# Performance work log

Measured on AMD Instinct MI355X. Metric: run time of the kernel, lower is better.

## Reference

```python
import jax, jax.numpy as jnp
import numpy as np

N = 50000      # nodes
E = 640000     # edges
FIN = 100      # raw node feature dim (nn.Linear(100, d_model))
D = 128        # d_model (dim_hidden)
H = 8          # num_heads
DH = D // H    # head dim
L = 4          # num_layers
DFF = 4 * D    # dim_feedforward
G = 64         # number of graphs in the batch
SCALE = DH ** -0.5


def setup_inputs() -> dict:
    key = jax.random.key(0)
    ks = jax.random.split(key, 12)
    x = jax.random.normal(ks[0], (N, FIN), jnp.float32)
    edge_index = jax.random.randint(ks[1], (2, E), 0, N, dtype=jnp.int64)
    batch = jnp.sort(jax.random.randint(ks[2], (N,), 0, G, dtype=jnp.int64))

    def w(k, shape, fan_in):
        return jax.random.normal(k, shape, jnp.float32) * (fan_in ** -0.5)

    W_embed = w(ks[3], (FIN, D), FIN)          # embedding, bias=False
    Wqk = w(ks[4], (L, D, 2 * D), D)           # to_qk, bias=False
    Wv = w(ks[5], (L, D, D), D)                # to_v, bias=False
    Wout = w(ks[6], (L, D, D), D)              # out_proj
    b_out = jnp.zeros((L, D), jnp.float32)
    W1 = w(ks[7], (L, D, DFF), D)              # FFN linear1
    b1 = jnp.zeros((L, DFF), jnp.float32)
    W2 = w(ks[8], (L, DFF, D), DFF)            # FFN linear2
    b2 = jnp.zeros((L, D), jnp.float32)
    return dict(x=x, edge_index=edge_index, batch=batch, W_embed=W_embed,
                Wqk=Wqk, Wv=Wv, Wout=Wout, b_out=b_out, W1=W1, b1=b1,
                W2=W2, b2=b2)


def reference(x, edge_index, batch, W_embed, Wqk, Wv, Wout, b_out, W1, b1, W2, b2):
    src = edge_index[0]  # j (message source)
    dst = edge_index[1]  # i (aggregation target)
    h = x @ W_embed  # [N, D]; dropout is identity at eval
    for l in range(L):
        # --- DAG multi-head attention (PyG MessagePassing, aggr='add') ---
        qk = h @ Wqk[l]
        q, k = qk[:, :D], qk[:, D:]
        v = h @ Wv[l]
        qj = q[src].reshape(E, H, DH)   # qk_j: gathered at source
        ki = k[dst].reshape(E, H, DH)   # qk_i: gathered at target
        logits = (qj * ki).sum(-1) * SCALE  # [E, H]
        # segment softmax over edges sharing the same target node
        m = jax.ops.segment_max(logits, dst, num_segments=N)        # [N, H]
        p = jnp.exp(logits - m[dst])
        ssum = jax.ops.segment_sum(p, dst, num_segments=N)          # [N, H]
        attn = p / ssum[dst]
        msg = (v[src].reshape(E, H, DH) * attn[:, :, None]).reshape(E, D)
        agg = jax.ops.segment_sum(msg, dst, num_segments=N)         # [N, D]
        h = h + (agg @ Wout[l] + b_out[l])   # residual; norm1 = Identity
        # --- FFN (relu) ---
        ff = jax.nn.relu(h @ W1[l] + b1[l]) @ W2[l] + b2[l]
        h = h + ff                            # residual; norm2 = Identity
    # global mean pool over graphs
    cnt = jax.ops.segment_sum(jnp.ones((N,), h.dtype), batch, num_segments=G)
    pooled = jax.ops.segment_sum(h, batch, num_segments=G) / jnp.maximum(cnt, 1.0)[:, None]
    return pooled
```

## Files before the change

### kernel.cpp

```cpp
#include <hip/hip_runtime.h>
#include <hip/hip_bf16.h>
#include <math.h>

#define D 128
#define NH 8
#define DFF 512
#define NG 64
#define NL 4
#define FIN 100
#define SCALE 0.25f
#define QKV 384

typedef __attribute__((ext_vector_type(8))) short short8;
typedef __attribute__((ext_vector_type(4))) float f32x4;

__device__ inline unsigned short f2bf(float v) {
    __hip_bfloat16 b = __float2bfloat16(v);
    return *reinterpret_cast<unsigned short*>(&b);
}

__global__ void count_kernel(const int* __restrict__ dst, int* __restrict__ cnt, int E) {
    int e = blockIdx.x * 256 + threadIdx.x;
    if (e < E) atomicAdd(&cnt[dst[e]], 1);
}

__global__ __launch_bounds__(1024) void scan_block_kernel(const int* __restrict__ cnt,
        int* __restrict__ incl, int* __restrict__ partials, int n) {
    __shared__ int s[1024];
    int tid = threadIdx.x;
    int gid = blockIdx.x * 1024 + tid;
    int val = (gid < n) ? cnt[gid] : 0;
    s[tid] = val;
    __syncthreads();
    for (int o = 1; o < 1024; o <<= 1) {
        int t = (tid >= o) ? s[tid - o] : 0;
        __syncthreads();
        s[tid] += t;
        __syncthreads();
    }
    if (gid < n) incl[gid] = s[tid];
    if (tid == 1023) partials[blockIdx.x] = s[1023];
}

__global__ void scan_partials_kernel(int* __restrict__ partials, int nb) {
    if (threadIdx.x == 0 && blockIdx.x == 0) {
        int run = 0;
        for (int i = 0; i < nb; ++i) { int t = partials[i]; partials[i] = run; run += t; }
    }
}

__global__ void finalize_off_kernel(const int* __restrict__ cnt, const int* __restrict__ incl,
        const int* __restrict__ partials, int* __restrict__ off, int* __restrict__ cur,
        int n, int E) {
    int gid = blockIdx.x * 256 + threadIdx.x;
    if (gid < n) {
        int v = incl[gid] - cnt[gid] + partials[gid >> 10];
        off[gid] = v;
        cur[gid] = v;
    }
    if (gid == 0) off[n] = E;
}

__global__ void scatter_kernel(const int* __restrict__ src, const int* __restrict__ dst,
        int* __restrict__ cur, int* __restrict__ csr_src, int E) {
    int e = blockIdx.x * 256 + threadIdx.x;
    if (e < E) {
        int p = atomicAdd(&cur[dst[e]], 1);
        csr_src[p] = src[e];
    }
}

__global__ void transpose_cvt_kernel(const float* __restrict__ W, __hip_bfloat16* __restrict__ Bt,
        int K, int N, int ldl) {
    int l = blockIdx.y;
    const float* w = W + (size_t)l * K * N;
    __hip_bfloat16* bt = Bt + (size_t)l * ldl;
    int idx = blockIdx.x * 256 + threadIdx.x;
    if (idx >= K * N) return;
    int n = idx / K, k = idx - n * K;
    bt[(size_t)n * K + k] = __float2bfloat16(w[(size_t)k * N + n]);
}

__global__ void pad_cvt_x_kernel(const float* __restrict__ x, __hip_bfloat16* __restrict__ xb, int n) {
    int idx = blockIdx.x * 256 + threadIdx.x;
    if (idx >= n * 128) return;
    int r = idx >> 7, c = idx & 127;
    xb[idx] = (c < FIN) ? __float2bfloat16(x[(size_t)r * FIN + c]) : __float2bfloat16(0.f);
}

__global__ void wembT_kernel(const float* __restrict__ W, __hip_bfloat16* __restrict__ Bt) {
    int idx = blockIdx.x * 256 + threadIdx.x;
    if (idx >= 128 * 128) return;
    int n = idx >> 7, k = idx & 127;
    Bt[idx] = (k < FIN) ? __float2bfloat16(W[(size_t)k * 128 + n]) : __float2bfloat16(0.f);
}

template<int EPI>
__global__ __launch_bounds__(256) void gemm_mfma(
        const __hip_bfloat16* __restrict__ A, const __hip_bfloat16* __restrict__ Bt,
        const float* __restrict__ bias,
        float* __restrict__ Cf, __hip_bfloat16* __restrict__ Cb,
        int M, int N, int K) {
    __shared__ __align__(16) unsigned short As[128][64];
    __shared__ __align__(16) unsigned short Bs[64][64];
    int t = threadIdx.x;
    int wave = t >> 6, lane = t & 63;
    int row0 = blockIdx.x * 128, col0 = blockIdx.y * 64;
    f32x4 acc[2][4] = {};

    int sr = t >> 3;
    int sc = t & 7;

    for (int k0 = 0; k0 < K; k0 += 64) {
#pragma unroll
        for (int i = 0; i < 4; ++i) {
            int r = i * 32 + sr;
            int gr = row0 + r;
            if (gr >= M) gr = M - 1;
            *reinterpret_cast<short8*>(&As[r][(sc ^ (r & 7)) << 3]) =
                *reinterpret_cast<const short8*>(&A[(size_t)gr * K + k0 + (sc << 3)]);
        }
#pragma unroll
        for (int i = 0; i < 2; ++i) {
            int r = i * 32 + sr;
            *reinterpret_cast<short8*>(&Bs[r][(sc ^ (r & 7)) << 3]) =
                *reinterpret_cast<const short8*>(&Bt[(size_t)(col0 + r) * K + k0 + (sc << 3)]);
        }
        __syncthreads();
#pragma unroll
        for (int kk = 0; kk < 64; kk += 32) {
            int lr = lane & 15;
            int kc = (kk >> 3) + (lane >> 4);
            short8 a[2], b[4];
#pragma unroll
            for (int m = 0; m < 2; ++m) {
                int r = wave * 32 + m * 16 + lr;
                a[m] = *reinterpret_cast<const short8*>(&As[r][(kc ^ (r & 7)) << 3]);
            }
#pragma unroll
            for (int n = 0; n < 4; ++n) {
                int r = n * 16 + lr;
                b[n] = *reinterpret_cast<const short8*>(&Bs[r][(kc ^ (r & 7)) << 3]);
            }
#pragma unroll
            for (int m = 0; m < 2; ++m)
#pragma unroll
                for (int n = 0; n < 4; ++n)
                    acc[m][n] = __builtin_amdgcn_mfma_f32_16x16x32_bf16(a[m], b[n], acc[m][n], 0, 0, 0);
        }
        __syncthreads();
    }

    int lr = lane & 15, rg = (lane >> 4) * 4;
#pragma unroll
    for (int m = 0; m < 2; ++m) {
#pragma unroll
        for (int n = 0; n < 4; ++n) {
            int col = col0 + n * 16 + lr;
#pragma unroll
            for (int j = 0; j < 4; ++j) {
                int row = row0 + wave * 32 + m * 16 + rg + j;
                if (row < M) {
                    float val = acc[m][n][j];
                    Cf[(size_t)row * N + col] = val;
                    Cb[(size_t)row * N + col] = __float2bfloat16(val);
                }
            }
        }
    }
}

__global__ __launch_bounds__(256, 3) void gemm_qkv(
        const __hip_bfloat16* __restrict__ A, const __hip_bfloat16* __restrict__ Bt,
        __hip_bfloat16* __restrict__ Cb, int M) {
    __shared__ __align__(16) unsigned short As[128 * 128];
    __shared__ __align__(16) unsigned short Bs[64 * 128];
    int t = threadIdx.x;
    int wave = t >> 6, lane = t & 63;
    int lr = lane & 15, lg = lane >> 4;
    int row0 = blockIdx.x * 128;

#pragma unroll
    for (int i = 0; i < 8; ++i) {
        int idx = t + i * 256;
        int r = idx >> 4, ch = idx & 15;
        int gr = row0 + r; if (gr >= M) gr = M - 1;
        *reinterpret_cast<short8*>(&As[r * 128 + ((ch ^ (r & 7)) << 3)]) =
            *reinterpret_cast<const short8*>(&A[(size_t)gr * 128 + ch * 8]);
    }

    short8 a_all[2][4];
    for (int c = 0; c < 6; ++c) {
#pragma unroll
        for (int i = 0; i < 4; ++i) {
            int idx = t + i * 256;
            int r = idx >> 4, ch = idx & 15;
            *reinterpret_cast<short8*>(&Bs[r * 128 + ((ch ^ (r & 7)) << 3)]) =
                *reinterpret_cast<const short8*>(&Bt[((size_t)(c * 64 + r)) * 128 + ch * 8]);
        }
        __syncthreads();
        if (c == 0) {
#pragma unroll
            for (int m = 0; m < 2; ++m)
#pragma unroll
                for (int ks = 0; ks < 4; ++ks) {
                    int r = wave * 32 + m * 16 + lr;
                    int kc = ks * 4 + lg;
                    a_all[m][ks] = *reinterpret_cast<const short8*>(&As[r * 128 + ((kc ^ (r & 7)) << 3)]);
                }
        }
        f32x4 acc[2][4] = {};
#pragma unroll
        for (int ks = 0; ks < 4; ++ks) {
            int kc = ks * 4 + lg;
            short8 b[4];
#pragma unroll
            for (int n = 0; n < 4; ++n) {
                int r = n * 16 + lr;
                b[n] = *reinterpret_cast<const short8*>(&Bs[r * 128 + ((kc ^ (r & 7)) << 3)]);
            }
#pragma unroll
            for (int m = 0; m < 2; ++m)
#pragma unroll
                for (int n = 0; n < 4; ++n)
                    acc[m][n] = __builtin_amdgcn_mfma_f32_16x16x32_bf16(a_all[m][ks], b[n], acc[m][n], 0, 0, 0);
        }
#pragma unroll
        for (int m = 0; m < 2; ++m)
#pragma unroll
            for (int n = 0; n < 4; ++n) {
                int col = c * 64 + n * 16 + lr;
#pragma unroll
                for (int j = 0; j < 4; ++j) {
                    int row = row0 + wave * 32 + m * 16 + lg * 4 + j;
                    if (row < M)
                        Cb[(size_t)row * QKV + col] = __float2bfloat16(acc[m][n][j]);
                }
            }
        __syncthreads();
    }
}

__global__ __launch_bounds__(256, 2) void fused_out_ffn(
        const __hip_bfloat16* __restrict__ aggb, const __hip_bfloat16* __restrict__ WoutT,
        const float* __restrict__ b_out,
        const __hip_bfloat16* __restrict__ W1T, const float* __restrict__ b1,
        const __hip_bfloat16* __restrict__ W2T, const float* __restrict__ b2,
        float* __restrict__ h32, __hip_bfloat16* __restrict__ hb, int M) {
    __shared__ __align__(16) unsigned short smem[32768];
    unsigned short* As   = smem;
    unsigned short* Bs   = smem + 16384;
    unsigned short* W1s  = smem;
    unsigned short* ff1s = smem + 8192;
    unsigned short* W2s  = smem + 16384;

    int t = threadIdx.x;
    int wave = t >> 6, lane = t & 63;
    int lr = lane & 15, lg = lane >> 4;
    int row0 = blockIdx.x * 128;

#pragma unroll
    for (int i = 0; i < 8; ++i) {
        int idx = t + i * 256;
        int r = idx >> 4, ch = idx & 15;
        int gr = row0 + r; if (gr >= M) gr = M - 1;
        *reinterpret_cast<short8*>(&As[r * 128 + ((ch ^ (r & 7)) << 3)]) =
            *reinterpret_cast<const short8*>(&aggb[(size_t)gr * 128 + ch * 8]);
        *reinterpret_cast<short8*>(&Bs[r * 128 + ((ch ^ (r & 7)) << 3)]) =
            *reinterpret_cast<const short8*>(&WoutT[(size_t)r * 128 + ch * 8]);
    }
    __syncthreads();

    f32x4 acc1[2][8] = {};
#pragma unroll
    for (int ks = 0; ks < 4; ++ks) {
        int kc = ks * 4 + lg;
        short8 a[2], b[8];
#pragma unroll
        for (int m = 0; m < 2; ++m) {
            int r = wave * 32 + m * 16 + lr;
            a[m] = *reinterpret_cast<const short8*>(&As[r * 128 + ((kc ^ (r & 7)) << 3)]);
        }
#pragma unroll
        for (int n = 0; n < 8; ++n) {
            int r = n * 16 + lr;
            b[n] = *reinterpret_cast<const short8*>(&Bs[r * 128 + ((kc ^ (r & 7)) << 3)]);
        }
#pragma unroll
        for (int m = 0; m < 2; ++m)
#pragma unroll
            for (int n = 0; n < 8; ++n)
                acc1[m][n] = __builtin_amdgcn_mfma_f32_16x16x32_bf16(a[m], b[n], acc1[m][n], 0, 0, 0);
    }

#pragma unroll
    for (int m = 0; m < 2; ++m) {
#pragma unroll
        for (int n = 0; n < 8; ++n) {
            int col = n * 16 + lr;
            float bo = b_out[col];
#pragma unroll
            for (int j = 0; j < 4; ++j) {
                int rl = wave * 32 + m * 16 + lg * 4 + j;
                int row = row0 + rl;
                float hv = (row < M) ? h32[(size_t)row * 128 + col] : 0.f;
                float val = acc1[m][n][j] + bo + hv;
                acc1[m][n][j] = val;
                float other = __shfl_xor(val, 1);
                if (!(lane & 1)) {
                    unsigned lo16 = f2bf(val), hi16 = f2bf(other);
                    int ch = col >> 3;
                    int addr = rl * 128 + ((ch ^ (rl & 7)) << 3) + (col & 7);
                    *reinterpret_cast<unsigned*>(&As[addr]) = lo16 | (hi16 << 16);
                }
            }
        }
    }

    short8 a_ff[2][4];
#pragma unroll
    for (int m = 0; m < 2; ++m)
#pragma unroll
        for (int ks = 0; ks < 4; ++ks) {
            int r = wave * 32 + m * 16 + lr;
            int kc = ks * 4 + lg;
            a_ff[m][ks] = *reinterpret_cast<const short8*>(&As[r * 128 + ((kc ^ (r & 7)) << 3)]);
        }
    __syncthreads();

    f32x4 h2acc[2][8] = {};
    for (int c = 0; c < 8; ++c) {
#pragma unroll
        for (int i = 0; i < 4; ++i) {
            int idx = t + i * 256;
            int r = idx >> 4, ch = idx & 15;
            *reinterpret_cast<short8*>(&W1s[r * 128 + ((ch ^ (r & 7)) << 3)]) =
                *reinterpret_cast<const short8*>(&W1T[((size_t)(c * 64 + r)) * 128 + ch * 8]);
        }
#pragma unroll
        for (int i = 0; i < 4; ++i) {
            int idx = t + i * 256;
            int r = idx >> 3, ch = idx & 7;
            *reinterpret_cast<short8*>(&W2s[r * 64 + ((ch ^ (r & 7)) << 3)]) =
                *reinterpret_cast<const short8*>(&W2T[(size_t)r * 512 + c * 64 + ch * 8]);
        }
        __syncthreads();

        f32x4 acc2[2][4] = {};
#pragma unroll
        for (int ks = 0; ks < 4; ++ks) {
            int kc = ks * 4 + lg;
            short8 b[4];
#pragma unroll
            for (int n = 0; n < 4; ++n) {
                int r = n * 16 + lr;
                b[n] = *reinterpret_cast<const short8*>(&W1s[r * 128 + ((kc ^ (r & 7)) << 3)]);
            }
#pragma unroll
            for (int m = 0; m < 2; ++m)
#pragma unroll
                for (int n = 0; n < 4; ++n)
                    acc2[m][n] = __builtin_amdgcn_mfma_f32_16x16x32_bf16(a_ff[m][ks], b[n], acc2[m][n], 0, 0, 0);
        }
#pragma unroll
        for (int m = 0; m < 2; ++m) {
#pragma unroll
            for (int n = 0; n < 4; ++n) {
                int col = n * 16 + lr;
                float bb = b1[c * 64 + col];
#pragma unroll
                for (int j = 0; j < 4; ++j) {
                    int rl = wave * 32 + m * 16 + lg * 4 + j;
                    float val = fmaxf(acc2[m][n][j] + bb, 0.f);
                    float other = __shfl_xor(val, 1);
                    if (!(lane & 1)) {
                        unsigned lo16 = f2bf(val), hi16 = f2bf(other);
                        int ch = col >> 3;
                        int addr = rl * 64 + ((ch ^ (rl & 7)) << 3) + (col & 7);
                        *reinterpret_cast<unsigned*>(&ff1s[addr]) = lo16 | (hi16 << 16);
                    }
                }
            }
        }
#pragma unroll
        for (int ks = 0; ks < 2; ++ks) {
            int kc = ks * 4 + lg;
            short8 a2[2], b[8];
#pragma unroll
            for (int m = 0; m < 2; ++m) {
                int r = wave * 32 + m * 16 + lr;
                a2[m] = *reinterpret_cast<const short8*>(&ff1s[r * 64 + ((kc ^ (r & 7)) << 3)]);
            }
#pragma unroll
            for (int n = 0; n < 8; ++n) {
                int r = n * 16 + lr;
                b[n] = *reinterpret_cast<const short8*>(&W2s[r * 64 + ((kc ^ (r & 7)) << 3)]);
            }
#pragma unroll
            for (int m = 0; m < 2; ++m)
#pragma unroll
                for (int n = 0; n < 8; ++n)
                    h2acc[m][n] = __builtin_amdgcn_mfma_f32_16x16x32_bf16(a2[m], b[n], h2acc[m][n], 0, 0, 0);
        }
        __syncthreads();
    }

#pragma unroll
    for (int m = 0; m < 2; ++m) {
#pragma unroll
        for (int n = 0; n < 8; ++n) {
            int col = n * 16 + lr;
            float bb = b2[col];
#pragma unroll
            for (int j = 0; j < 4; ++j) {
                int row = row0 + wave * 32 + m * 16 + lg * 4 + j;
                if (row < M) {
                    float val = acc1[m][n][j] + h2acc[m][n][j] + bb;
                    h32[(size_t)row * 128 + col] = val;
                    hb[(size_t)row * 128 + col] = __float2bfloat16(val);
                }
            }
        }
    }
}

__global__ __launch_bounds__(256) void attn_kernel(const __hip_bfloat16* __restrict__ qkvb,
        const int* __restrict__ off, const int* __restrict__ csr_src,
        __hip_bfloat16* __restrict__ aggb, int n) {
    int wave = threadIdx.x >> 6;
    int lane = threadIdx.x & 63;
    int i = blockIdx.x * 4 + wave;
    if (i >= n) return;
    const unsigned* qv = reinterpret_cast<const unsigned*>(qkvb);
    unsigned ku = qv[(size_t)i * 192 + 64 + lane];
    float kx = __uint_as_float(ku << 16);
    float ky = __uint_as_float(ku & 0xffff0000u);
    int e0 = off[i], e1 = off[i + 1];
    float m = -INFINITY, ssum = 0.f, ax = 0.f, ay = 0.f;
    int e = e0;
    for (; e + 4 <= e1; e += 4) {
        int s0 = csr_src[e], s1 = csr_src[e + 1], s2 = csr_src[e + 2], s3 = csr_src[e + 3];
        unsigned q0 = qv[(size_t)s0 * 192 + lane];
        unsigned q1 = qv[(size_t)s1 * 192 + lane];
        unsigned q2 = qv[(size_t)s2 * 192 + lane];
        unsigned q3 = qv[(size_t)s3 * 192 + lane];
        unsigned w0 = qv[(size_t)s0 * 192 + 128 + lane];
        unsigned w1 = qv[(size_t)s1 * 192 + 128 + lane];
        unsigned w2 = qv[(size_t)s2 * 192 + 128 + lane];
        unsigned w3 = qv[(size_t)s3 * 192 + 128 + lane];
        float l0 = __uint_as_float(q0 << 16) * kx + __uint_as_float(q0 & 0xffff0000u) * ky;
        float l1 = __uint_as_float(q1 << 16) * kx + __uint_as_float(q1 & 0xffff0000u) * ky;
        float l2 = __uint_as_float(q2 << 16) * kx + __uint_as_float(q2 & 0xffff0000u) * ky;
        float l3 = __uint_as_float(q3 << 16) * kx + __uint_as_float(q3 & 0xffff0000u) * ky;
        l0 += __shfl_xor(l0, 1); l1 += __shfl_xor(l1, 1); l2 += __shfl_xor(l2, 1); l3 += __shfl_xor(l3, 1);
        l0 += __shfl_xor(l0, 2); l1 += __shfl_xor(l1, 2); l2 += __shfl_xor(l2, 2); l3 += __shfl_xor(l3, 2);
        l0 += __shfl_xor(l0, 4); l1 += __shfl_xor(l1, 4); l2 += __shfl_xor(l2, 4); l3 += __shfl_xor(l3, 4);
        l0 *= SCALE; l1 *= SCALE; l2 *= SCALE; l3 *= SCALE;
        float mx = fmaxf(fmaxf(l0, l1), fmaxf(l2, l3));
        float mn = fmaxf(m, mx);
        float corr = __expf(m - mn);
        float p0 = __expf(l0 - mn);
        float p1 = __expf(l1 - mn);
        float p2 = __expf(l2 - mn);
        float p3 = __expf(l3 - mn);
        ssum = ssum * corr + ((p0 + p1) + (p2 + p3));
        ax = ax * corr + p0 * __uint_as_float(w0 << 16) + p1 * __uint_as_float(w1 << 16)
                       + p2 * __uint_as_float(w2 << 16) + p3 * __uint_as_float(w3 << 16);
        ay = ay * corr + p0 * __uint_as_float(w0 & 0xffff0000u) + p1 * __uint_as_float(w1 & 0xffff0000u)
                       + p2 * __uint_as_float(w2 & 0xffff0000u) + p3 * __uint_as_float(w3 & 0xffff0000u);
        m = mn;
    }
    for (; e < e1; ++e) {
        int s0 = csr_src[e];
        unsigned q0 = qv[(size_t)s0 * 192 + lane];
        unsigned w0 = qv[(size_t)s0 * 192 + 128 + lane];
        float l0 = __uint_as_float(q0 << 16) * kx + __uint_as_float(q0 & 0xffff0000u) * ky;
// ... 69 lines not shown

    int Nn = in_sizes[2];
    int E = in_sizes[1] / 2;

    char* p = (char*)d_ws;
    auto alloc = [&](size_t bytes) {
        char* r = p;
        p += (bytes + 255) & ~(size_t)255;
        return r;
    };
    float* h32 = (float*)alloc((size_t)Nn * D * 4);
    __hip_bfloat16* hb = (__hip_bfloat16*)alloc((size_t)Nn * D * 2);
    __hip_bfloat16* aggb = (__hip_bfloat16*)alloc((size_t)Nn * D * 2);
    __hip_bfloat16* qkvb = (__hip_bfloat16*)alloc((size_t)Nn * QKV * 2);
    __hip_bfloat16* xb = (__hip_bfloat16*)alloc((size_t)Nn * D * 2);
    __hip_bfloat16* WembT = (__hip_bfloat16*)alloc((size_t)D * D * 2);
    __hip_bfloat16* WqkvT = (__hip_bfloat16*)alloc((size_t)NL * QKV * D * 2);
    __hip_bfloat16* WoutT = (__hip_bfloat16*)alloc((size_t)NL * D * D * 2);
    __hip_bfloat16* W1T = (__hip_bfloat16*)alloc((size_t)NL * D * DFF * 2);
    __hip_bfloat16* W2T = (__hip_bfloat16*)alloc((size_t)NL * DFF * D * 2);
    int* csr_src = (int*)alloc((size_t)E * 4);
    int* cnt = (int*)alloc((size_t)Nn * 4);
    int* incl = (int*)alloc((size_t)Nn * 4);
    int* off = (int*)alloc(((size_t)Nn + 1) * 4);
    int* cur = (int*)alloc((size_t)Nn * 4);
    int* partials = (int*)alloc(1024 * 4);
    int* gstart = (int*)alloc((NG + 1) * 4);
    float* pws = (float*)alloc((size_t)NG * 8 * 128 * 4);

    const int* e_src = ei;
    const int* e_dst = ei + E;

    hipMemsetAsync(cnt, 0, (size_t)Nn * 4, stream);
    count_kernel<<<(E + 255) / 256, 256, 0, stream>>>(e_dst, cnt, E);
    int nsb = (Nn + 1023) / 1024;
    scan_block_kernel<<<nsb, 1024, 0, stream>>>(cnt, incl, partials, Nn);
    scan_partials_kernel<<<1, 64, 0, stream>>>(partials, nsb);
    finalize_off_kernel<<<(Nn + 255) / 256, 256, 0, stream>>>(cnt, incl, partials, off, cur, Nn, E);
    scatter_kernel<<<(E + 255) / 256, 256, 0, stream>>>(e_src, e_dst, cur, csr_src, E);

    transpose_cvt_kernel<<<dim3((2 * D * D + 255) / 256, NL), 256, 0, stream>>>(
        Wqk, WqkvT, D, 2 * D, QKV * D);
    transpose_cvt_kernel<<<dim3((D * D + 255) / 256, NL), 256, 0, stream>>>(
        Wv, WqkvT + (size_t)2 * D * D, D, D, QKV * D);
    transpose_cvt_kernel<<<dim3((D * D + 255) / 256, NL), 256, 0, stream>>>(
        Wout, WoutT, D, D, D * D);
    transpose_cvt_kernel<<<dim3((D * DFF + 255) / 256, NL), 256, 0, stream>>>(
        W1, W1T, D, DFF, D * DFF);
    transpose_cvt_kernel<<<dim3((DFF * D + 255) / 256, NL), 256, 0, stream>>>(
        W2, W2T, DFF, D, DFF * D);
    wembT_kernel<<<(128 * 128 + 255) / 256, 256, 0, stream>>>(W_embed, WembT);
    pad_cvt_x_kernel<<<((size_t)Nn * 128 + 255) / 256, 256, 0, stream>>>(x, xb, Nn);

    int gmb = (Nn + 127) / 128;
    gemm_mfma<3><<<dim3(gmb, D / 64), 256, 0, stream>>>(
        xb, WembT, nullptr, h32, hb, Nn, D, D);

    for (int l = 0; l < NL; ++l) {
        gemm_qkv<<<gmb, 256, 0, stream>>>(hb, WqkvT + (size_t)l * QKV * D, qkvb, Nn);
        attn_kernel<<<(Nn + 3) / 4, 256, 0, stream>>>(qkvb, off, csr_src, aggb, Nn);
        fused_out_ffn<<<gmb, 256, 0, stream>>>(
            aggb, WoutT + (size_t)l * D * D, b_out + (size_t)l * D,
            W1T + (size_t)l * D * DFF, b1 + (size_t)l * DFF,
            W2T + (size_t)l * DFF * D, b2 + (size_t)l * D,
            h32, hb, Nn);
    }

    group_bounds_kernel<<<1, 128, 0, stream>>>(batch, Nn, gstart);
    pool_stage1<<<dim3(NG, 8), 256, 0, stream>>>(h32, gstart, pws);
    pool_stage2<<<NG, 128, 0, stream>>>(pws, gstart, (float*)d_out);
}
```

Measured before the change: 700.4 us.

## Load GEMM operands directly from global memory, dropping LDS staging and block syncs

The embed, QKV and fused out-proj/FFN GEMMs now load A and B fragments straight from global memory into registers instead of staging tiles in shared memory behind __syncthreads. The FFN keeps only small per-wave LDS buffers for re-layout and synchronises with s_waitcnt rather than block barriers. It also drops the separate h2acc accumulator by accumulating into acc1, which lowers register pressure and removes the min-blocks launch bound. The goal is to remove barrier stalls and LDS traffic. The cost is redundant global and L2 reads of the weights by every wave, plus uncoalesced fragment loads.

```diff
diff --git a/kernel.cpp b/kernel.cpp
--- a/kernel.cpp
+++ b/kernel.cpp
@@ -95,135 +95,80 @@
     Bt[idx] = (k < FIN) ? __float2bfloat16(W[(size_t)k * 128 + n]) : __float2bfloat16(0.f);
 }
 
-template<int EPI>
-__global__ __launch_bounds__(256) void gemm_mfma(
+__global__ __launch_bounds__(256) void embed_kernel(
         const __hip_bfloat16* __restrict__ A, const __hip_bfloat16* __restrict__ Bt,
-        const float* __restrict__ bias,
-        float* __restrict__ Cf, __hip_bfloat16* __restrict__ Cb,
-        int M, int N, int K) {
-    __shared__ __align__(16) unsigned short As[128][64];
-    __shared__ __align__(16) unsigned short Bs[64][64];
-    int t = threadIdx.x;
-    int wave = t >> 6, lane = t & 63;
-    int row0 = blockIdx.x * 128, col0 = blockIdx.y * 64;
-    f32x4 acc[2][4] = {};
-
-    int sr = t >> 3;
-    int sc = t & 7;
-
-    for (int k0 = 0; k0 < K; k0 += 64) {
-#pragma unroll
-        for (int i = 0; i < 4; ++i) {
-            int r = i * 32 + sr;
-            int gr = row0 + r;
-            if (gr >= M) gr = M - 1;
-            *reinterpret_cast<short8*>(&As[r][(sc ^ (r & 7)) << 3]) =
-                *reinterpret_cast<const short8*>(&A[(size_t)gr * K + k0 + (sc << 3)]);
-        }
-#pragma unroll
-        for (int i = 0; i < 2; ++i) {
-            int r = i * 32 + sr;
-            *reinterpret_cast<short8*>(&Bs[r][(sc ^ (r & 7)) << 3]) =
-                *reinterpret_cast<const short8*>(&Bt[(size_t)(col0 + r) * K + k0 + (sc << 3)]);
-        }
-        __syncthreads();
-#pragma unroll
-        for (int kk = 0; kk < 64; kk += 32) {
-            int lr = lane & 15;
-            int kc = (kk >> 3) + (lane >> 4);
-            short8 a[2], b[4];
-#pragma unroll
-            for (int m = 0; m < 2; ++m) {
-                int r = wave * 32 + m * 16 + lr;
-                a[m] = *reinterpret_cast<const short8*>(&As[r][(kc ^ (r & 7)) << 3]);
-            }
-#pragma unroll
-            for (int n = 0; n < 4; ++n) {
-                int r = n * 16 + lr;
-                b[n] = *reinterpret_cast<const short8*>(&Bs[r][(kc ^ (r & 7)) << 3]);
-            }
-#pragma unroll
-            for (int m = 0; m < 2; ++m)
-#pragma unroll
-                for (int n = 0; n < 4; ++n)
-                    acc[m][n] = __builtin_amdgcn_mfma_f32_16x16x32_bf16(a[m], b[n], acc[m][n], 0, 0, 0);
-        }
-        __syncthreads();
-    }
-
-    int lr = lane & 15, rg = (lane >> 4) * 4;
-#pragma unroll
-    for (int m = 0; m < 2; ++m) {
-#pragma unroll
-        for (int n = 0; n < 4; ++n) {
-            int col = col0 + n * 16 + lr;
-#pragma unroll
-            for (int j = 0; j < 4; ++j) {
-                int row = row0 + wave * 32 + m * 16 + rg + j;
-                if (row < M) {
-                    float val = acc[m][n][j];
-                    Cf[(size_t)row * N + col] = val;
-                    Cb[(size_t)row * N + col] = __float2bfloat16(val);
-                }
-            }
-        }
-    }
-}
-
-__global__ __launch_bounds__(256, 3) void gemm_qkv(
-        const __hip_bfloat16* __restrict__ A, const __hip_bfloat16* __restrict__ Bt,
-        __hip_bfloat16* __restrict__ Cb, int M) {
-    __shared__ __align__(16) unsigned short As[128 * 128];
-    __shared__ __align__(16) unsigned short Bs[64 * 128];
+        float* __restrict__ h32, __hip_bfloat16* __restrict__ hb, int M) {
     int t = threadIdx.x;
     int wave = t >> 6, lane = t & 63;
     int lr = lane & 15, lg = lane >> 4;
-    int row0 = blockIdx.x * 128;
-
-#pragma unroll
-    for (int i = 0; i < 8; ++i) {
-        int idx = t + i * 256;
-        int r = idx >> 4, ch = idx & 15;
-        int gr = row0 + r; if (gr >= M) gr = M - 1;
-        *reinterpret_cast<short8*>(&As[r * 128 + ((ch ^ (r & 7)) << 3)]) =
-            *reinterpret_cast<const short8*>(&A[(size_t)gr * 128 + ch * 8]);
-    }
-
-    short8 a_all[2][4];
+    int row0 = blockIdx.x * 128 + wave * 32;
+    f32x4 acc[2][8] = {};
+#pragma unroll
+    for (int ks = 0; ks < 4; ++ks) {
+        int kc = ks * 4 + lg;
+        short8 a[2], b[8];
+#pragma unroll
+        for (int m = 0; m < 2; ++m) {
+            int gr = row0 + m * 16 + lr; if (gr >= M) gr = M - 1;
+            a[m] = *reinterpret_cast<const short8*>(&A[(size_t)gr * 128 + kc * 8]);
+        }
+#pragma unroll
+        for (int n = 0; n < 8; ++n)
+            b[n] = *reinterpret_cast<const short8*>(&Bt[(size_t)(n * 16 + lr) * 128 + kc * 8]);
+#pragma unroll
+        for (int m = 0; m < 2; ++m)
+#pragma unroll
+            for (int n = 0; n < 8; ++n)
+                acc[m][n] = __builtin_amdgcn_mfma_f32_16x16x32_bf16(a[m], b[n], acc[m][n], 0, 0, 0);
+    }
+#pragma unroll
+    for (int m = 0; m < 2; ++m)
+#pragma unroll
+        for (int n = 0; n < 8; ++n) {
+            int col = n * 16 + lr;
+#pragma unroll
+            for (int j = 0; j < 4; ++j) {
+                int row = row0 + m * 16 + lg * 4 + j;
+                if (row < M) {
+                    float val = acc[m][n][j];
+                    h32[(size_t)row * 128 + col] = val;
+                    hb[(size_t)row * 128 + col] = __float2bfloat16(val);
+                }
+            }
+        }
+}
+
+__global__ __launch_bounds__(256) void gemm_qkv(
+        const __hip_bfloat16* __restrict__ A, const __hip_bfloat16* __restrict__ Bt,
+        __hip_bfloat16* __restrict__ Cb, int M) {
+    int t = threadIdx.x;
+    int wave = t >> 6, lane = t & 63;
+    int lr = lane & 15, lg = lane >> 4;
+    int row0 = blockIdx.x * 128 + wave * 32;
+
+    short8 a[2][4];
+#pragma unroll
+    for (int m = 0; m < 2; ++m)
+#pragma unroll
+        for (int ks = 0; ks < 4; ++ks) {
+            int gr = row0 + m * 16 + lr; if (gr >= M) gr = M - 1;
+            a[m][ks] = *reinterpret_cast<const short8*>(&A[(size_t)gr * 128 + (ks * 4 + lg) * 8]);
+        }
+
     for (int c = 0; c < 6; ++c) {
-#pragma unroll
-        for (int i = 0; i < 4; ++i) {
-            int idx = t + i * 256;
-            int r = idx >> 4, ch = idx & 15;
-            *reinterpret_cast<short8*>(&Bs[r * 128 + ((ch ^ (r & 7)) << 3)]) =
-                *reinterpret_cast<const short8*>(&Bt[((size_t)(c * 64 + r)) * 128 + ch * 8]);
-        }
-        __syncthreads();
-        if (c == 0) {
-#pragma unroll
-            for (int m = 0; m < 2; ++m)
-#pragma unroll
-                for (int ks = 0; ks < 4; ++ks) {
-                    int r = wave * 32 + m * 16 + lr;
-                    int kc = ks * 4 + lg;
-                    a_all[m][ks] = *reinterpret_cast<const short8*>(&As[r * 128 + ((kc ^ (r & 7)) << 3)]);
-                }
-        }
         f32x4 acc[2][4] = {};
 #pragma unroll
         for (int ks = 0; ks < 4; ++ks) {
             int kc = ks * 4 + lg;
             short8 b[4];
 #pragma unroll
-            for (int n = 0; n < 4; ++n) {
-                int r = n * 16 + lr;
-                b[n] = *reinterpret_cast<const short8*>(&Bs[r * 128 + ((kc ^ (r & 7)) << 3)]);
-            }
+            for (int n = 0; n < 4; ++n)
+                b[n] = *reinterpret_cast<const short8*>(&Bt[(size_t)(c * 64 + n * 16 + lr) * 128 + kc * 8]);
 #pragma unroll
             for (int m = 0; m < 2; ++m)
 #pragma unroll
                 for (int n = 0; n < 4; ++n)
-                    acc[m][n] = __builtin_amdgcn_mfma_f32_16x16x32_bf16(a_all[m][ks], b[n], acc[m][n], 0, 0, 0);
+                    acc[m][n] = __builtin_amdgcn_mfma_f32_16x16x32_bf16(a[m][ks], b[n], acc[m][n], 0, 0, 0);
         }
 #pragma unroll
         for (int m = 0; m < 2; ++m)
@@ -232,44 +177,29 @@
                 int col = c * 64 + n * 16 + lr;
 #pragma unroll
                 for (int j = 0; j < 4; ++j) {
-                    int row = row0 + wave * 32 + m * 16 + lg * 4 + j;
+                    int row = row0 + m * 16 + lg * 4 + j;
                     if (row < M)
                         Cb[(size_t)row * QKV + col] = __float2bfloat16(acc[m][n][j]);
                 }
             }
-        __syncthreads();
-    }
-}
-
-__global__ __launch_bounds__(256, 2) void fused_out_ffn(
+    }
+}
+
+__global__ __launch_bounds__(256) void fused_out_ffn(
         const __hip_bfloat16* __restrict__ aggb, const __hip_bfloat16* __restrict__ WoutT,
         const float* __restrict__ b_out,
         const __hip_bfloat16* __restrict__ W1T, const float* __restrict__ b1,
         const __hip_bfloat16* __restrict__ W2T, const float* __restrict__ b2,
         float* __restrict__ h32, __hip_bfloat16* __restrict__ hb, int M) {
-    __shared__ __align__(16) unsigned short smem[32768];
-    unsigned short* As   = smem;
-    unsigned short* Bs   = smem + 16384;
-    unsigned short* W1s  = smem;
-    unsigned short* ff1s = smem + 8192;
-    unsigned short* W2s  = smem + 16384;
+    __shared__ __align__(16) unsigned short hT[4][32 * 128];
+    __shared__ __align__(16) unsigned short f1[4][32 * 64];
 
     int t = threadIdx.x;
     int wave = t >> 6, lane = t & 63;
     int lr = lane & 15, lg = lane >> 4;
-    int row0 = blockIdx.x * 128;
-
-#pragma unroll
-    for (int i = 0; i < 8; ++i) {
-        int idx = t + i * 256;
-        int r = idx >> 4, ch = idx & 15;
-        int gr = row0 + r; if (gr >= M) gr = M - 1;
-        *reinterpret_cast<short8*>(&As[r * 128 + ((ch ^ (r & 7)) << 3)]) =
-            *reinterpret_cast<const short8*>(&aggb[(size_t)gr * 128 + ch * 8]);
-        *reinterpret_cast<short8*>(&Bs[r * 128 + ((ch ^ (r & 7)) << 3)]) =
-            *reinterpret_cast<const short8*>(&WoutT[(size_t)r * 128 + ch * 8]);
-    }
-    __syncthreads();
+    int row0 = blockIdx.x * 128 + wave * 32;
+    unsigned short* hw = hT[wave];
+    unsigned short* fw = f1[wave];
 
     f32x4 acc1[2][8] = {};
 #pragma unroll
@@ -278,14 +208,12 @@
         short8 a[2], b[8];
 #pragma unroll
         for (int m = 0; m < 2; ++m) {
-            int r = wave * 32 + m * 16 + lr;
-            a[m] = *reinterpret_cast<const short8*>(&As[r * 128 + ((kc ^ (r & 7)) << 3)]);
-        }
-#pragma unroll
-        for (int n = 0; n < 8; ++n) {
-            int r = n * 16 + lr;
-            b[n] = *reinterpret_cast<const short8*>(&Bs[r * 128 + ((kc ^ (r & 7)) << 3)]);
-        }
+            int gr = row0 + m * 16 + lr; if (gr >= M) gr = M - 1;
+            a[m] = *reinterpret_cast<const short8*>(&aggb[(size_t)gr * 128 + kc * 8]);
+        }
+#pragma unroll
+        for (int n = 0; n < 8; ++n)
+            b[n] = *reinterpret_cast<const short8*>(&WoutT[(size_t)(n * 16 + lr) * 128 + kc * 8]);
 #pragma unroll
         for (int m = 0; m < 2; ++m)
 #pragma unroll
@@ -294,68 +222,48 @@
     }
 
 #pragma unroll
-    for (int m = 0; m < 2; ++m) {
+    for (int m = 0; m < 2; ++m)
 #pragma unroll
         for (int n = 0; n < 8; ++n) {
             int col = n * 16 + lr;
             float bo = b_out[col];
 #pragma unroll
             for (int j = 0; j < 4; ++j) {
-                int rl = wave * 32 + m * 16 + lg * 4 + j;
+                int rl = m * 16 + lg * 4 + j;
                 int row = row0 + rl;
                 float hv = (row < M) ? h32[(size_t)row * 128 + col] : 0.f;
                 float val = acc1[m][n][j] + bo + hv;
                 acc1[m][n][j] = val;
                 float other = __shfl_xor(val, 1);
                 if (!(lane & 1)) {
-                    unsigned lo16 = f2bf(val), hi16 = f2bf(other);
+                    unsigned pack = (unsigned)f2bf(val) | ((unsigned)f2bf(other) << 16);
                     int ch = col >> 3;
                     int addr = rl * 128 + ((ch ^ (rl & 7)) << 3) + (col & 7);
-                    *reinterpret_cast<unsigned*>(&As[addr]) = lo16 | (hi16 << 16);
+                    *reinterpret_cast<unsigned*>(&hw[addr]) = pack;
                 }
             }
         }
-    }
+    asm volatile("s_waitcnt lgkmcnt(0)" ::: "memory");
 
     short8 a_ff[2][4];
 #pragma unroll
     for (int m = 0; m < 2; ++m)
 #pragma unroll
         for (int ks = 0; ks < 4; ++ks) {
-            int r = wave * 32 + m * 16 + lr;
+            int r = m * 16 + lr;
             int kc = ks * 4 + lg;
-            a_ff[m][ks] = *reinterpret_cast<const short8*>(&As[r * 128 + ((kc ^ (r & 7)) << 3)]);
-        }
-    __syncthreads();
-
-    f32x4 h2acc[2][8] = {};
+            a_ff[m][ks] = *reinterpret_cast<const short8*>(&hw[r * 128 + ((kc ^ (r & 7)) << 3)]);
+        }
+
     for (int c = 0; c < 8; ++c) {
-#pragma unroll
-        for (int i = 0; i < 4; ++i) {
-            int idx = t + i * 256;
-            int r = idx >> 4, ch = idx & 15;
-            *reinterpret_cast<short8*>(&W1s[r * 128 + ((ch ^ (r & 7)) << 3)]) =
-                *reinterpret_cast<const short8*>(&W1T[((size_t)(c * 64 + r)) * 128 + ch * 8]);
-        }
-#pragma unroll
-        for (int i = 0; i < 4; ++i) {
-            int idx = t + i * 256;
-            int r = idx >> 3, ch = idx & 7;
-            *reinterpret_cast<short8*>(&W2s[r * 64 + ((ch ^ (r & 7)) << 3)]) =
-                *reinterpret_cast<const short8*>(&W2T[(size_t)r * 512 + c * 64 + ch * 8]);
-        }
-        __syncthreads();
-
         f32x4 acc2[2][4] = {};
 #pragma unroll
         for (int ks = 0; ks < 4; ++ks) {
             int kc = ks * 4 + lg;
             short8 b[4];
 #pragma unroll
-            for (int n = 0; n < 4; ++n) {
-                int r = n * 16 + lr;
-                b[n] = *reinterpret_cast<const short8*>(&W1s[r * 128 + ((kc ^ (r & 7)) << 3)]);
-            }
+            for (int n = 0; n < 4; ++n)
+                b[n] = *reinterpret_cast<const short8*>(&W1T[(size_t)(c * 64 + n * 16 + lr) * 128 + kc * 8]);
 #pragma unroll
             for (int m = 0; m < 2; ++m)
 #pragma unroll
@@ -363,65 +271,61 @@
                     acc2[m][n] = __builtin_amdgcn_mfma_f32_16x16x32_bf16(a_ff[m][ks], b[n], acc2[m][n], 0, 0, 0);
         }
 #pragma unroll
-        for (int m = 0; m < 2; ++m) {
+        for (int m = 0; m < 2; ++m)
 #pragma unroll
             for (int n = 0; n < 4; ++n) {
-                int col = n * 16 + lr;
-                float bb = b1[c * 64 + col];
+                int colc = n * 16 + lr;
+                float bb = b1[c * 64 + colc];
 #pragma unroll
                 for (int j = 0; j < 4; ++j) {
-                    int rl = wave * 32 + m * 16 + lg * 4 + j;
+                    int rl = m * 16 + lg * 4 + j;
                     float val = fmaxf(acc2[m][n][j] + bb, 0.f);
                     float other = __shfl_xor(val, 1);
                     if (!(lane & 1)) {
-                        unsigned lo16 = f2bf(val), hi16 = f2bf(other);
-                        int ch = col >> 3;
-                        int addr = rl * 64 + ((ch ^ (rl & 7)) << 3) + (col & 7);
-                        *reinterpret_cast<unsigned*>(&ff1s[addr]) = lo16 | (hi16 << 16);
+                        unsigned pack = (unsigned)f2bf(val) | ((unsigned)f2bf(other) << 16);
+                        int ch = colc >> 3;
+                        int addr = rl * 64 + ((ch ^ (rl & 7)) << 3) + (colc & 7);
+                        *reinterpret_cast<unsigned*>(&fw[addr]) = pack;
                     }
                 }
             }
-        }
+        asm volatile("s_waitcnt lgkmcnt(0)" ::: "memory");
 #pragma unroll
         for (int ks = 0; ks < 2; ++ks) {
             int kc = ks * 4 + lg;
             short8 a2[2], b[8];
 #pragma unroll
             for (int m = 0; m < 2; ++m) {
-                int r = wave * 32 + m * 16 + lr;
-                a2[m] = *reinterpret_cast<const short8*>(&ff1s[r * 64 + ((kc ^ (r & 7)) << 3)]);
+                int r = m * 16 + lr;
+                a2[m] = *reinterpret_cast<const short8*>(&fw[r * 64 + ((kc ^ (r & 7)) << 3)]);
             }
 #pragma unroll
-            for (int n = 0; n < 8; ++n) {
-                int r = n * 16 + lr;
-                b[n] = *reinterpret_cast<const short8*>(&W2s[r * 64 + ((kc ^ (r & 7)) << 3)]);
-            }
+            for (int n = 0; n < 8; ++n)
+                b[n] = *reinterpret_cast<const short8*>(&W2T[(size_t)(n * 16 + lr) * 512 + c * 64 + kc * 8]);
 #pragma unroll
             for (int m = 0; m < 2; ++m)
 #pragma unroll
                 for (int n = 0; n < 8; ++n)
-                    h2acc[m][n] = __builtin_amdgcn_mfma_f32_16x16x32_bf16(a2[m], b[n], h2acc[m][n], 0, 0, 0);
-        }
-        __syncthreads();
-    }
-
-#pragma unroll
-    for (int m = 0; m < 2; ++m) {
+                    acc1[m][n] = __builtin_amdgcn_mfma_f32_16x16x32_bf16(a2[m], b[n], acc1[m][n], 0, 0, 0);
+        }
+    }
+
+#pragma unroll
+    for (int m = 0; m < 2; ++m)
 #pragma unroll
         for (int n = 0; n < 8; ++n) {
             int col = n * 16 + lr;
             float bb = b2[col];
 #pragma unroll
             for (int j = 0; j < 4; ++j) {
-                int row = row0 + wave * 32 + m * 16 + lg * 4 + j;
+                int row = row0 + m * 16 + lg * 4 + j;
                 if (row < M) {
-                    float val = acc1[m][n][j] + h2acc[m][n][j] + bb;
+                    float val = acc1[m][n][j] + bb;
                     h32[(size_t)row * 128 + col] = val;
                     hb[(size_t)row * 128 + col] = __float2bfloat16(val);
                 }
             }
         }
-    }
 }
 
 __global__ __launch_bounds__(256) void attn_kernel(const __hip_bfloat16* __restrict__ qkvb,
@@ -598,8 +502,7 @@
     pad_cvt_x_kernel<<<((size_t)Nn * 128 + 255) / 256, 256, 0, stream>>>(x, xb, Nn);
 
     int gmb = (Nn + 127) / 128;
-    gemm_mfma<3><<<dim3(gmb, D / 64), 256, 0, stream>>>(
-        xb, WembT, nullptr, h32, hb, Nn, D, D);
+    embed_kernel<<<gmb, 256, 0, stream>>>(xb, WembT, h32, hb, Nn);
 
     for (int l = 0; l < NL; ++l) {
         gemm_qkv<<<gmb, 256, 0, stream>>>(hb, WqkvT + (size_t)l * QKV * D, qkvb, Nn);
```

Result: slower. 1.043 ms (+49.0%).

## Shrink QKV and fused FFN row tiles to 64 with per-wave private ff1 buffers

Applied to the files above, without the earlier changes.

Both the QKV GEMM and the fused out-proj+FFN kernel now process 64-row tiles instead of 128, so each wave handles 16 rows and the grid doubles. The FFN kernel stores its ReLU intermediate in a per-wave slice of shared memory, which lets it skip a block barrier between the two GEMMs and accumulate the second GEMM directly into the residual accumulator. Register and LDS use per block drop, which should raise occupancy and parallelism. The cost is that weight tiles are reloaded from global/L2 twice as often per row, and the MFMA-to-LDS-read ratio is lower.

```diff
diff --git a/kernel.cpp b/kernel.cpp
--- a/kernel.cpp
+++ b/kernel.cpp
@@ -14,9 +14,9 @@
 typedef __attribute__((ext_vector_type(8))) short short8;
 typedef __attribute__((ext_vector_type(4))) float f32x4;
 
-__device__ inline unsigned short f2bf(float v) {
+__device__ inline unsigned f2bf(float v) {
     __hip_bfloat16 b = __float2bfloat16(v);
-    return *reinterpret_cast<unsigned short*>(&b);
+    return (unsigned)*reinterpret_cast<unsigned short*>(&b);
 }
 
 __global__ void count_kernel(const int* __restrict__ dst, int* __restrict__ cnt, int E) {
@@ -95,10 +95,8 @@
     Bt[idx] = (k < FIN) ? __float2bfloat16(W[(size_t)k * 128 + n]) : __float2bfloat16(0.f);
 }
 
-template<int EPI>
 __global__ __launch_bounds__(256) void gemm_mfma(
         const __hip_bfloat16* __restrict__ A, const __hip_bfloat16* __restrict__ Bt,
-        const float* __restrict__ bias,
         float* __restrict__ Cf, __hip_bfloat16* __restrict__ Cb,
         int M, int N, int K) {
     __shared__ __align__(16) unsigned short As[128][64];
@@ -170,255 +168,235 @@
     }
 }
 
-__global__ __launch_bounds__(256, 3) void gemm_qkv(
+__global__ __launch_bounds__(256) void gemm_qkv(
         const __hip_bfloat16* __restrict__ A, const __hip_bfloat16* __restrict__ Bt,
         __hip_bfloat16* __restrict__ Cb, int M) {
-    __shared__ __align__(16) unsigned short As[128 * 128];
+    __shared__ __align__(16) unsigned short As[64 * 128];
     __shared__ __align__(16) unsigned short Bs[64 * 128];
     int t = threadIdx.x;
     int wave = t >> 6, lane = t & 63;
     int lr = lane & 15, lg = lane >> 4;
-    int row0 = blockIdx.x * 128;
-
-#pragma unroll
-    for (int i = 0; i < 8; ++i) {
+    int row0 = blockIdx.x * 64;
+    int wrow = wave * 16;
+
+#pragma unroll
+    for (int i = 0; i < 4; ++i) {
         int idx = t + i * 256;
         int r = idx >> 4, ch = idx & 15;
         int gr = row0 + r; if (gr >= M) gr = M - 1;
         *reinterpret_cast<short8*>(&As[r * 128 + ((ch ^ (r & 7)) << 3)]) =
             *reinterpret_cast<const short8*>(&A[(size_t)gr * 128 + ch * 8]);
-    }
-
-    short8 a_all[2][4];
+        *reinterpret_cast<short8*>(&Bs[r * 128 + ((ch ^ (r & 7)) << 3)]) =
+            *reinterpret_cast<const short8*>(&Bt[(size_t)r * 128 + ch * 8]);
+    }
+    __syncthreads();
+
+    short8 a[4];
+#pragma unroll
+    for (int ks = 0; ks < 4; ++ks) {
+        int r = wrow + lr;
+        int kc = ks * 4 + lg;
+        a[ks] = *reinterpret_cast<const short8*>(&As[r * 128 + ((kc ^ (r & 7)) << 3)]);
+    }
+
     for (int c = 0; c < 6; ++c) {
-#pragma unroll
-        for (int i = 0; i < 4; ++i) {
-            int idx = t + i * 256;
-            int r = idx >> 4, ch = idx & 15;
-            *reinterpret_cast<short8*>(&Bs[r * 128 + ((ch ^ (r & 7)) << 3)]) =
-                *reinterpret_cast<const short8*>(&Bt[((size_t)(c * 64 + r)) * 128 + ch * 8]);
-        }
-        __syncthreads();
-        if (c == 0) {
-#pragma unroll
-            for (int m = 0; m < 2; ++m)
-#pragma unroll
-                for (int ks = 0; ks < 4; ++ks) {
-                    int r = wave * 32 + m * 16 + lr;
-                    int kc = ks * 4 + lg;
-                    a_all[m][ks] = *reinterpret_cast<const short8*>(&As[r * 128 + ((kc ^ (r & 7)) << 3)]);
-                }
-        }
-        f32x4 acc[2][4] = {};
+        f32x4 acc[4] = {};
 #pragma unroll
         for (int ks = 0; ks < 4; ++ks) {
             int kc = ks * 4 + lg;
             short8 b[4];
 #pragma unroll
             for (int n = 0; n < 4; ++n) {
-                int r = n * 16 + lr;
-                b[n] = *reinterpret_cast<const short8*>(&Bs[r * 128 + ((kc ^ (r & 7)) << 3)]);
-            }
-#pragma unroll
-            for (int m = 0; m < 2; ++m)
-#pragma unroll
-                for (int n = 0; n < 4; ++n)
-                    acc[m][n] = __builtin_amdgcn_mfma_f32_16x16x32_bf16(a_all[m][ks], b[n], acc[m][n], 0, 0, 0);
-        }
-#pragma unroll
-        for (int m = 0; m < 2; ++m)
-#pragma unroll
-            for (int n = 0; n < 4; ++n) {
-                int col = c * 64 + n * 16 + lr;
-#pragma unroll
-                for (int j = 0; j < 4; ++j) {
-                    int row = row0 + wave * 32 + m * 16 + lg * 4 + j;
-                    if (row < M)
-                        Cb[(size_t)row * QKV + col] = __float2bfloat16(acc[m][n][j]);
-                }
-            }
-        __syncthreads();
-    }
-}
-
-__global__ __launch_bounds__(256, 2) void fused_out_ffn(
+                int br = n * 16 + lr;
+                b[n] = *reinterpret_cast<const short8*>(&Bs[br * 128 + ((kc ^ (br & 7)) << 3)]);
+            }
+#pragma unroll
+            for (int n = 0; n < 4; ++n)
+                acc[n] = __builtin_amdgcn_mfma_f32_16x16x32_bf16(a[ks], b[n], acc[n], 0, 0, 0);
+        }
+#pragma unroll
+        for (int n = 0; n < 4; ++n) {
+            int col = c * 64 + n * 16 + lr;
+#pragma unroll
+            for (int j = 0; j < 4; ++j) {
+                int row = row0 + wrow + lg * 4 + j;
+                if (row < M)
+                    Cb[(size_t)row * QKV + col] = __float2bfloat16(acc[n][j]);
+            }
+        }
+        if (c < 5) {
+            __syncthreads();
+#pragma unroll
+            for (int i = 0; i < 4; ++i) {
+                int idx = t + i * 256;
+                int r = idx >> 4, ch = idx & 15;
+                *reinterpret_cast<short8*>(&Bs[r * 128 + ((ch ^ (r & 7)) << 3)]) =
+                    *reinterpret_cast<const short8*>(&Bt[((size_t)((c + 1) * 64 + r)) * 128 + ch * 8]);
+            }
+            __syncthreads();
+        }
+    }
+}
+
+__global__ __launch_bounds__(256) void fused_out_ffn(
         const __hip_bfloat16* __restrict__ aggb, const __hip_bfloat16* __restrict__ WoutT,
         const float* __restrict__ b_out,
         const __hip_bfloat16* __restrict__ W1T, const float* __restrict__ b1,
         const __hip_bfloat16* __restrict__ W2T, const float* __restrict__ b2,
         float* __restrict__ h32, __hip_bfloat16* __restrict__ hb, int M) {
-    __shared__ __align__(16) unsigned short smem[32768];
-    unsigned short* As   = smem;
-    unsigned short* Bs   = smem + 16384;
-    unsigned short* W1s  = smem;
-    unsigned short* ff1s = smem + 8192;
-    unsigned short* W2s  = smem + 16384;
+    __shared__ __align__(16) unsigned short R0[64 * 128];
+    __shared__ __align__(16) unsigned short R1[128 * 128];
+    unsigned short* W1c = R1;
+    unsigned short* W2c = R1 + 8192;
 
     int t = threadIdx.x;
     int wave = t >> 6, lane = t & 63;
     int lr = lane & 15, lg = lane >> 4;
-    int row0 = blockIdx.x * 128;
-
+    int row0 = blockIdx.x * 64;
+    int wrow = wave * 16;
+
+#pragma unroll
+    for (int i = 0; i < 4; ++i) {
+        int idx = t + i * 256;
+        int r = idx >> 4, ch = idx & 15;
+        int gr = row0 + r; if (gr >= M) gr = M - 1;
+        *reinterpret_cast<short8*>(&R0[r * 128 + ((ch ^ (r & 7)) << 3)]) =
+            *reinterpret_cast<const short8*>(&aggb[(size_t)gr * 128 + ch * 8]);
+    }
 #pragma unroll
     for (int i = 0; i < 8; ++i) {
         int idx = t + i * 256;
         int r = idx >> 4, ch = idx & 15;
-        int gr = row0 + r; if (gr >= M) gr = M - 1;
-        *reinterpret_cast<short8*>(&As[r * 128 + ((ch ^ (r & 7)) << 3)]) =
-            *reinterpret_cast<const short8*>(&aggb[(size_t)gr * 128 + ch * 8]);
-        *reinterpret_cast<short8*>(&Bs[r * 128 + ((ch ^ (r & 7)) << 3)]) =
+        *reinterpret_cast<short8*>(&R1[r * 128 + ((ch ^ (r & 7)) << 3)]) =
             *reinterpret_cast<const short8*>(&WoutT[(size_t)r * 128 + ch * 8]);
     }
     __syncthreads();
 
-    f32x4 acc1[2][8] = {};
+    f32x4 acc1[8] = {};
 #pragma unroll
     for (int ks = 0; ks < 4; ++ks) {
         int kc = ks * 4 + lg;
-        short8 a[2], b[8];
-#pragma unroll
-        for (int m = 0; m < 2; ++m) {
-            int r = wave * 32 + m * 16 + lr;
-            a[m] = *reinterpret_cast<const short8*>(&As[r * 128 + ((kc ^ (r & 7)) << 3)]);
-        }
+        int ar = wrow + lr;
+        short8 a = *reinterpret_cast<const short8*>(&R0[ar * 128 + ((kc ^ (ar & 7)) << 3)]);
+        short8 b[8];
 #pragma unroll
         for (int n = 0; n < 8; ++n) {
-            int r = n * 16 + lr;
-            b[n] = *reinterpret_cast<const short8*>(&Bs[r * 128 + ((kc ^ (r & 7)) << 3)]);
-        }
-#pragma unroll
-        for (int m = 0; m < 2; ++m)
-#pragma unroll
-            for (int n = 0; n < 8; ++n)
-                acc1[m][n] = __builtin_amdgcn_mfma_f32_16x16x32_bf16(a[m], b[n], acc1[m][n], 0, 0, 0);
-    }
-
-#pragma unroll
-    for (int m = 0; m < 2; ++m) {
-#pragma unroll
-        for (int n = 0; n < 8; ++n) {
-            int col = n * 16 + lr;
-            float bo = b_out[col];
-#pragma unroll
-            for (int j = 0; j < 4; ++j) {
-                int rl = wave * 32 + m * 16 + lg * 4 + j;
-                int row = row0 + rl;
-                float hv = (row < M) ? h32[(size_t)row * 128 + col] : 0.f;
-                float val = acc1[m][n][j] + bo + hv;
-                acc1[m][n][j] = val;
-                float other = __shfl_xor(val, 1);
-                if (!(lane & 1)) {
-                    unsigned lo16 = f2bf(val), hi16 = f2bf(other);
-                    int ch = col >> 3;
-                    int addr = rl * 128 + ((ch ^ (rl & 7)) << 3) + (col & 7);
-                    *reinterpret_cast<unsigned*>(&As[addr]) = lo16 | (hi16 << 16);
-                }
-            }
-        }
-    }
-
-    short8 a_ff[2][4];
-#pragma unroll
-    for (int m = 0; m < 2; ++m)
-#pragma unroll
-        for (int ks = 0; ks < 4; ++ks) {
-            int r = wave * 32 + m * 16 + lr;
-            int kc = ks * 4 + lg;
-            a_ff[m][ks] = *reinterpret_cast<const short8*>(&As[r * 128 + ((kc ^ (r & 7)) << 3)]);
-        }
+            int br = n * 16 + lr;
+            b[n] = *reinterpret_cast<const short8*>(&R1[br * 128 + ((kc ^ (br & 7)) << 3)]);
+        }
+#pragma unroll
+        for (int n = 0; n < 8; ++n)
+            acc1[n] = __builtin_amdgcn_mfma_f32_16x16x32_bf16(a, b[n], acc1[n], 0, 0, 0);
+    }
+
+#pragma unroll
+    for (int n = 0; n < 8; ++n) {
+        int col = n * 16 + lr;
+        float bo = b_out[col];
+#pragma unroll
+        for (int j = 0; j < 4; ++j) {
+            int rl = wrow + lg * 4 + j;
+            int row = row0 + rl;
+            float hv = (row < M) ? h32[(size_t)row * 128 + col] : 0.f;
+            float val = acc1[n][j] + bo + hv;
+            acc1[n][j] = val;
+            float other = __shfl_xor(val, 1);
+            if (!(lane & 1)) {
+                unsigned pack = f2bf(val) | (f2bf(other) << 16);
+                int ch = col >> 3;
+                *reinterpret_cast<unsigned*>(&R0[rl * 128 + ((ch ^ (rl & 7)) << 3) + (col & 7)]) = pack;
+            }
+        }
+    }
+    asm volatile("s_waitcnt lgkmcnt(0)" ::: "memory");
+
+    short8 a_ff[4];
+#pragma unroll
+    for (int ks = 0; ks < 4; ++ks) {
+        int r = wrow + lr;
+        int kc = ks * 4 + lg;
+        a_ff[ks] = *reinterpret_cast<const short8*>(&R0[r * 128 + ((kc ^ (r & 7)) << 3)]);
+    }
     __syncthreads();
 
-    f32x4 h2acc[2][8] = {};
+    unsigned short* fw = R0 + wrow * 128;
     for (int c = 0; c < 8; ++c) {
 #pragma unroll
         for (int i = 0; i < 4; ++i) {
             int idx = t + i * 256;
             int r = idx >> 4, ch = idx & 15;
-            *reinterpret_cast<short8*>(&W1s[r * 128 + ((ch ^ (r & 7)) << 3)]) =
+            *reinterpret_cast<short8*>(&W1c[r * 128 + ((ch ^ (r & 7)) << 3)]) =
                 *reinterpret_cast<const short8*>(&W1T[((size_t)(c * 64 + r)) * 128 + ch * 8]);
         }
 #pragma unroll
         for (int i = 0; i < 4; ++i) {
             int idx = t + i * 256;
             int r = idx >> 3, ch = idx & 7;
-            *reinterpret_cast<short8*>(&W2s[r * 64 + ((ch ^ (r & 7)) << 3)]) =
+            *reinterpret_cast<short8*>(&W2c[r * 64 + ((ch ^ (r & 7)) << 3)]) =
                 *reinterpret_cast<const short8*>(&W2T[(size_t)r * 512 + c * 64 + ch * 8]);
         }
         __syncthreads();
 
-        f32x4 acc2[2][4] = {};
+        f32x4 acc2[4] = {};
 #pragma unroll
         for (int ks = 0; ks < 4; ++ks) {
             int kc = ks * 4 + lg;
             short8 b[4];
 #pragma unroll
             for (int n = 0; n < 4; ++n) {
-                int r = n * 16 + lr;
-                b[n] = *reinterpret_cast<const short8*>(&W1s[r * 128 + ((kc ^ (r & 7)) << 3)]);
-            }
-#pragma unroll
-            for (int m = 0; m < 2; ++m)
-#pragma unroll
-                for (int n = 0; n < 4; ++n)
-                    acc2[m][n] = __builtin_amdgcn_mfma_f32_16x16x32_bf16(a_ff[m][ks], b[n], acc2[m][n], 0, 0, 0);
-        }
-#pragma unroll
-        for (int m = 0; m < 2; ++m) {
-#pragma unroll
-            for (int n = 0; n < 4; ++n) {
-                int col = n * 16 + lr;
-                float bb = b1[c * 64 + col];
-#pragma unroll
-                for (int j = 0; j < 4; ++j) {
-                    int rl = wave * 32 + m * 16 + lg * 4 + j;
-                    float val = fmaxf(acc2[m][n][j] + bb, 0.f);
-                    float other = __shfl_xor(val, 1);
-                    if (!(lane & 1)) {
-                        unsigned lo16 = f2bf(val), hi16 = f2bf(other);
-                        int ch = col >> 3;
-                        int addr = rl * 64 + ((ch ^ (rl & 7)) << 3) + (col & 7);
-                        *reinterpret_cast<unsigned*>(&ff1s[addr]) = lo16 | (hi16 << 16);
-                    }
+                int br = n * 16 + lr;
+                b[n] = *reinterpret_cast<const short8*>(&W1c[br * 128 + ((kc ^ (br & 7)) << 3)]);
+            }
+#pragma unroll
+            for (int n = 0; n < 4; ++n)
+                acc2[n] = __builtin_amdgcn_mfma_f32_16x16x32_bf16(a_ff[ks], b[n], acc2[n], 0, 0, 0);
+        }
+#pragma unroll
+        for (int n = 0; n < 4; ++n) {
+            int colc = n * 16 + lr;
+            float bb = b1[c * 64 + colc];
+#pragma unroll
+            for (int j = 0; j < 4; ++j) {
+                int rl = lg * 4 + j;
+                float val = fmaxf(acc2[n][j] + bb, 0.f);
+                float other = __shfl_xor(val, 1);
+                if (!(lane & 1)) {
+                    unsigned pack = f2bf(val) | (f2bf(other) << 16);
+                    int ch = colc >> 3;
+                    *reinterpret_cast<unsigned*>(&fw[rl * 64 + ((ch ^ (rl & 7)) << 3) + (colc & 7)]) = pack;
                 }
             }
         }
+        asm volatile("s_waitcnt lgkmcnt(0)" ::: "memory");
 #pragma unroll
         for (int ks = 0; ks < 2; ++ks) {
             int kc = ks * 4 + lg;
-            short8 a2[2], b[8];
-#pragma unroll
-            for (int m = 0; m < 2; ++m) {
-                int r = wave * 32 + m * 16 + lr;
-                a2[m] = *reinterpret_cast<const short8*>(&ff1s[r * 64 + ((kc ^ (r & 7)) << 3)]);
-            }
+            int ar = lr;
+            short8 a2 = *reinterpret_cast<const short8*>(&fw[ar * 64 + ((kc ^ (ar & 7)) << 3)]);
+            short8 b[8];
 #pragma unroll
             for (int n = 0; n < 8; ++n) {
-                int r = n * 16 + lr;
-                b[n] = *reinterpret_cast<const short8*>(&W2s[r * 64 + ((kc ^ (r & 7)) << 3)]);
-            }
-#pragma unroll
-            for (int m = 0; m < 2; ++m)
-#pragma unroll
-                for (int n = 0; n < 8; ++n)
-                    h2acc[m][n] = __builtin_amdgcn_mfma_f32_16x16x32_bf16(a2[m], b[n], h2acc[m][n], 0, 0, 0);
+                int br = n * 16 + lr;
+                b[n] = *reinterpret_cast<const short8*>(&W2c[br * 64 + ((kc ^ (br & 7)) << 3)]);
+            }
+#pragma unroll
+            for (int n = 0; n < 8; ++n)
+                acc1[n] = __builtin_amdgcn_mfma_f32_16x16x32_bf16(a2, b[n], acc1[n], 0, 0, 0);
         }
         __syncthreads();
     }
 
 #pragma unroll
-    for (int m = 0; m < 2; ++m) {
-#pragma unroll
-        for (int n = 0; n < 8; ++n) {
-            int col = n * 16 + lr;
-            float bb = b2[col];
-#pragma unroll
-            for (int j = 0; j < 4; ++j) {
-                int row = row0 + wave * 32 + m * 16 + lg * 4 + j;
-                if (row < M) {
-                    float val = acc1[m][n][j] + h2acc[m][n][j] + bb;
-                    h32[(size_t)row * 128 + col] = val;
-                    hb[(size_t)row * 128 + col] = __float2bfloat16(val);
-                }
+    for (int n = 0; n < 8; ++n) {
+        int col = n * 16 + lr;
+        float bb = b2[col];
+#pragma unroll
+        for (int j = 0; j < 4; ++j) {
+            int row = row0 + wrow + lg * 4 + j;
+            if (row < M) {
+                float val = acc1[n][j] + bb;
+                h32[(size_t)row * 128 + col] = val;
+                hb[(size_t)row * 128 + col] = __float2bfloat16(val);
             }
         }
     }
@@ -597,14 +575,14 @@
     wembT_kernel<<<(128 * 128 + 255) / 256, 256, 0, stream>>>(W_embed, WembT);
     pad_cvt_x_kernel<<<((size_t)Nn * 128 + 255) / 256, 256, 0, stream>>>(x, xb, Nn);
 
-    int gmb = (Nn + 127) / 128;
-    gemm_mfma<3><<<dim3(gmb, D / 64), 256, 0, stream>>>(
-        xb, WembT, nullptr, h32, hb, Nn, D, D);
+    int gmb128 = (Nn + 127) / 128;
+    int gmb64 = (Nn + 63) / 64;
+    gemm_mfma<<<dim3(gmb128, D / 64), 256, 0, stream>>>(xb, WembT, h32, hb, Nn, D, D);
 
     for (int l = 0; l < NL; ++l) {
-        gemm_qkv<<<gmb, 256, 0, stream>>>(hb, WqkvT + (size_t)l * QKV * D, qkvb, Nn);
+        gemm_qkv<<<gmb64, 256, 0, stream>>>(hb, WqkvT + (size_t)l * QKV * D, qkvb, Nn);
         attn_kernel<<<(Nn + 3) / 4, 256, 0, stream>>>(qkvb, off, csr_src, aggb, Nn);
-        fused_out_ffn<<<gmb, 256, 0, stream>>>(
+        fused_out_ffn<<<gmb64, 256, 0, stream>>>(
             aggb, WoutT + (size_t)l * D * D, b_out + (size_t)l * D,
             W1T + (size_t)l * D * DFF, b1 + (size_t)l * DFF,
             W2T + (size_t)l * DFF * D, b2 + (size_t)l * D,
```

Result: slower. 811.5 us (+15.9%).
